# Performance work log

Measured on AMD Instinct MI355X. Metric: run time of the kernel, lower is better.

The kernel has to match this reference:

```python
import jax, jax.numpy as jnp
import numpy as np

IUNITS = 64  # input channels; scale is sqrt(iunits), per the original code


def setup_inputs() -> dict:
    key = jax.random.key(0)
    ks = jax.random.split(key, 4)
    B, N, Cin, Cout = 16, 2048, 64, 128
    x = jax.random.normal(ks[0], (B, N, Cin), dtype=jnp.float32)
    # 0.05 scaling keeps naive exp/sum softmax in a sane numeric range
    Wq = jax.random.normal(ks[1], (Cin, Cout), dtype=jnp.float32) * 0.05
    Wk = jax.random.normal(ks[2], (Cin, Cout), dtype=jnp.float32) * 0.05
    Wv = jax.random.normal(ks[3], (Cin, Cout), dtype=jnp.float32) * 0.05
    bq = jnp.zeros((Cout,), dtype=jnp.float32)
    bk = jnp.zeros((Cout,), dtype=jnp.float32)
    bv = jnp.zeros((Cout,), dtype=jnp.float32)
    return {"x": x, "Wq": Wq, "bq": bq, "Wk": Wk, "bk": bk, "Wv": Wv, "bv": bv}


def reference(x, Wq, bq, Wk, bk, Wv, bv):
    # Dense projections with ReLU activation (as in the original Dense(..., activation='relu'))
    Q = jax.nn.relu(jnp.einsum('bnc,cd->bnd', x, Wq) + bq)  # [B,N,D]
    K = jax.nn.relu(jnp.einsum('bnc,cd->bnd', x, Wk) + bk)  # [B,N,D]
    V = jax.nn.relu(jnp.einsum('bnc,cd->bnd', x, Wv) + bv)  # [B,N,D]
    scale = jnp.sqrt(jnp.float32(IUNITS))  # NOTE: sqrt of INPUT units, per source
    qk = jnp.einsum('bnd,bmd->bnm', Q, K) / scale            # [B,N,N]
    # exp/sum softmax over last axis; jax.nn.softmax is the same math, stabilized
    wgts = jax.nn.softmax(qk, axis=-1)
    return jnp.einsum('bnm,bmd->bnd', wgts, V)               # [B,N,D]
```

## Files before the change

### kernel.cpp

```cpp
#include <hip/hip_runtime.h>

typedef unsigned short u16;
typedef unsigned int u32;
typedef __bf16 bf16x8 __attribute__((ext_vector_type(8)));
typedef float f32x16 __attribute__((ext_vector_type(16)));
typedef u32 u32x4 __attribute__((ext_vector_type(4)));

#define QSCALE 0.18033688011112042f

__device__ __forceinline__ u16 bfbits(float f) {
  __bf16 h = (__bf16)f;
  return __builtin_bit_cast(u16, h);
}
__device__ __forceinline__ u32 pack2(float lo, float hi) {
  return (u32)bfbits(lo) | ((u32)bfbits(hi) << 16);
}
__device__ __forceinline__ void pl32swap(u32& a, u32& b) {
  asm volatile("v_permlane32_swap_b32 %0, %1" : "+v"(a), "+v"(b));
}
__device__ __forceinline__ void gload_lds16(const void* g, void* l) {
  __builtin_amdgcn_global_load_lds(
      (const __attribute__((address_space(1))) void*)g,
      (__attribute__((address_space(3))) void*)l, 16, 0, 0);
}

__global__ __launch_bounds__(256) void kv_proj_kernel(
    const float* __restrict__ x,
    const float* __restrict__ Wk, const float* __restrict__ bk,
    const float* __restrict__ Wv, const float* __restrict__ bv,
    u16* __restrict__ Kb, u16* __restrict__ VbT) {
  __shared__ __align__(16) u16 xs[64 * 64];
  const int t = threadIdx.x, w = t >> 6, lane = t & 63;
  const int ql = lane & 31, hi = lane >> 5;
  const int ws_ = w & 1;
  const int th = w >> 1;
  const size_t rg0 = (size_t)blockIdx.x * 64;

  {
    const float4* xsrc = reinterpret_cast<const float4*>(x + rg0 * 64);
#pragma unroll
    for (int i = 0; i < 4; ++i) {
      int idx = t + i * 256;
      int row = idx >> 4, c4 = idx & 15;
      float4 v = xsrc[idx];
      char* p = reinterpret_cast<char*>(xs) + row * 128 + ((c4 * 8) ^ ((row & 7) << 4));
      *reinterpret_cast<uint2*>(p) = make_uint2(pack2(v.x, v.y), pack2(v.z, v.w));
    }
  }
  __syncthreads();

  bf16x8 xf[4];
  {
    const int row = ws_ * 32 + ql;
    const char* base = reinterpret_cast<const char*>(xs) + row * 128;
    const int swz = (row & 7) << 4;
#pragma unroll
    for (int j = 0; j < 4; ++j)
      xf[j] = *reinterpret_cast<const bf16x8*>(base + ((j * 32 + hi * 16) ^ swz));
  }

  const float* W = th ? Wv : Wk;
  const float* bb = th ? bv : bk;
  const int b = (int)(rg0 >> 11);
  const int n0 = (int)(rg0 & 2047);

#pragma unroll
  for (int ct = 0; ct < 4; ++ct) {
    const int c = ct * 32 + ql;
    f32x16 acc;
#pragma unroll
    for (int i2 = 0; i2 < 16; ++i2) acc[i2] = 0.f;
#pragma unroll
    for (int j = 0; j < 4; ++j) {
      u32 wp[4];
#pragma unroll
      for (int e2 = 0; e2 < 4; ++e2) {
        float w0 = W[(j * 16 + hi * 8 + 2 * e2) * 128 + c];
        float w1 = W[(j * 16 + hi * 8 + 2 * e2 + 1) * 128 + c];
        wp[e2] = pack2(w0, w1);
      }
      u32x4 ww; ww.x = wp[0]; ww.y = wp[1]; ww.z = wp[2]; ww.w = wp[3];
      const bf16x8 wf = __builtin_bit_cast(bf16x8, ww);
      acc = __builtin_amdgcn_mfma_f32_32x32x16_bf16(xf[j], wf, acc, 0, 0, 0);
    }
    const float bias = bb[c];
    if (th == 0) {
#pragma unroll
      for (int reg = 0; reg < 16; ++reg) {
        const int i = (reg & 3) + 8 * (reg >> 2) + 4 * hi;
        Kb[(rg0 + ws_ * 32 + i) * 128 + c] = bfbits(fmaxf(acc[reg] + bias, 0.f));
      }
    } else {
      u16* vrow = VbT + ((size_t)(b * 128 + c)) * 2048;
#pragma unroll
      for (int g2 = 0; g2 < 4; ++g2) {
        u32 p0 = pack2(fmaxf(acc[4 * g2 + 0] + bias, 0.f),
                       fmaxf(acc[4 * g2 + 1] + bias, 0.f));
        u32 p1 = pack2(fmaxf(acc[4 * g2 + 2] + bias, 0.f),
                       fmaxf(acc[4 * g2 + 3] + bias, 0.f));
        const int n = n0 + ws_ * 32 + 8 * g2 + 4 * hi;
        *reinterpret_cast<uint2*>(vrow + n) = make_uint2(p0, p1);
      }
    }
  }
}

__global__ __launch_bounds__(256) void attn_kernel(
    const float* __restrict__ x,
    const float* __restrict__ Wq, const float* __restrict__ bq,
    const u16* __restrict__ Kb, const u16* __restrict__ VbT,
    float* __restrict__ out) {
  __shared__ __align__(16) char smem[65536];

  const int bid = ((int)blockIdx.x & 7) * 64 + ((int)blockIdx.x >> 3);
  const int b = bid >> 5;
  const int qt = bid & 31;
  const int t = threadIdx.x, w = t >> 6, lane = t & 63;
  const int ql = lane & 31, hi = lane >> 5;
  const size_t rg0 = (size_t)b * 2048 + qt * 64;
  const int sw = (ql & 7) << 4;

  {
    u16* xs = reinterpret_cast<u16*>(smem + 16384);
    const float4* xsrc = reinterpret_cast<const float4*>(x + rg0 * 64);
#pragma unroll
    for (int i = 0; i < 4; ++i) {
      int idx = t + i * 256;
      int row = idx >> 4, c4 = idx & 15;
      float4 v = xsrc[idx];
      char* p = reinterpret_cast<char*>(xs) + row * 128 + ((c4 * 8) ^ ((row & 7) << 4));
      *reinterpret_cast<uint2*>(p) = make_uint2(pack2(v.x, v.y), pack2(v.z, v.w));
    }
    __syncthreads();

    const int ws_ = w & 1;
    bf16x8 xf[4];
    {
      const int row = ws_ * 32 + ql;
      const char* base = reinterpret_cast<const char*>(xs) + row * 128;
      const int swz = (row & 7) << 4;
#pragma unroll
      for (int j = 0; j < 4; ++j)
        xf[j] = *reinterpret_cast<const bf16x8*>(base + ((j * 32 + hi * 16) ^ swz));
    }
#pragma unroll
    for (int u = 0; u < 2; ++u) {
      const int ct = (w >> 1) * 2 + u;
      const int c = ct * 32 + ql;
      f32x16 acc;
#pragma unroll
      for (int i2 = 0; i2 < 16; ++i2) acc[i2] = 0.f;
#pragma unroll
      for (int j = 0; j < 4; ++j) {
        u32 wp[4];
#pragma unroll
        for (int e2 = 0; e2 < 4; ++e2) {
          float w0 = Wq[(j * 16 + hi * 8 + 2 * e2) * 128 + c];
          float w1 = Wq[(j * 16 + hi * 8 + 2 * e2 + 1) * 128 + c];
          wp[e2] = pack2(w0, w1);
        }
        u32x4 ww; ww.x = wp[0]; ww.y = wp[1]; ww.z = wp[2]; ww.w = wp[3];
        const bf16x8 wf = __builtin_bit_cast(bf16x8, ww);
        acc = __builtin_amdgcn_mfma_f32_32x32x16_bf16(xf[j], wf, acc, 0, 0, 0);
      }
      const float bias = bq[c];
#pragma unroll
      for (int reg = 0; reg < 16; ++reg) {
        const int i = (reg & 3) + 8 * (reg >> 2) + 4 * hi;
        const int r = ws_ * 32 + i;
        *reinterpret_cast<u16*>(smem + r * 256 + ((2 * c) ^ ((r & 7) << 4))) =
            bfbits(fmaxf(acc[reg] + bias, 0.f) * QSCALE);
      }
    }
  }
  __syncthreads();

  const int qw = w >> 1, par = w & 1;
  const int q0 = qt * 64 + qw * 32;
  bf16x8 qf[8];
  {
    const int r = qw * 32 + ql;
    const char* base = smem + r * 256;
    const int swz = (r & 7) << 4;
#pragma unroll
    for (int f = 0; f < 8; ++f)
      qf[f] = *reinterpret_cast<const bf16x8*>(base + ((f * 32 + hi * 16) ^ swz));
  }
  __syncthreads();

  f32x16 Oacc[4], lacc;
#pragma unroll
  for (int i = 0; i < 16; ++i) {
    Oacc[0][i] = 0.f; Oacc[1][i] = 0.f; Oacc[2][i] = 0.f; Oacc[3][i] = 0.f;
    lacc[i] = 0.f;
  }
  u32x4 ow; ow.x = ow.y = ow.z = ow.w = 0x3F803F80u;
  const bf16x8 ones = __builtin_bit_cast(bf16x8, ow);

  const u16* Kbase = Kb + (size_t)b * 2048 * 128;
  const u16* Vbase = VbT + (size_t)b * 128 * 2048;

  const u16* kgp[4]; const u16* vgp[4];
  int ldso[4];
#pragma unroll
  for (int i = 0; i < 4; ++i) {
    const int Lb = (w * 4 + i) * 1024 + lane * 16;
    ldso[i] = (w * 4 + i) * 1024;
    const int kr = Lb >> 8;
    const int ks = ((Lb >> 4) & 15) ^ (kr & 7);
    kgp[i] = Kbase + kr * 128 + ks * 8;
    const int vr = Lb >> 7;
    const int vs = ((Lb >> 4) & 7) ^ (vr & 7);
    vgp[i] = Vbase + (size_t)vr * 2048 + vs * 8;
  }

#pragma unroll
  for (int i = 0; i < 4; ++i) {
    gload_lds16(kgp[i], smem + ldso[i]);
    gload_lds16(vgp[i], smem + 32768 + ldso[i]);
  }
  __syncthreads();

  for (int ss = 0; ss < 32; ++ss) {
    const int cur = ss & 1;
    if (ss < 31) {
      const size_t ko = (size_t)(ss + 1) * 8192;
      const int vo = (ss + 1) * 64;
      const int bo = (cur ^ 1) * 16384;
#pragma unroll
      for (int i = 0; i < 4; ++i) {
        gload_lds16(kgp[i] + ko, smem + bo + ldso[i]);
        gload_lds16(vgp[i] + vo, smem + 32768 + bo + ldso[i]);
      }
    }
    const char* kb0 = smem + cur * 16384;
    const char* vb0 = smem + 32768 + cur * 16384;

    f32x16 s0;
#pragma unroll
    for (int i = 0; i < 16; ++i) s0[i] = 0.f;
    const char* kbp = kb0 + (par * 32 + ql) * 256;
    __builtin_amdgcn_s_setprio(1);
#pragma unroll
    for (int f = 0; f < 8; ++f) {
      bf16x8 k0 = *reinterpret_cast<const bf16x8*>(kbp + ((f * 32 + hi * 16) ^ sw));
      s0 = __builtin_amdgcn_mfma_f32_32x32x16_bf16(k0, qf[f], s0, 0, 0, 0);
    }
    __builtin_amdgcn_s_setprio(0);

    u32 pk[8];
#pragma unroll
    for (int m = 0; m < 8; ++m)
      pk[m] = pack2(__builtin_amdgcn_exp2f(s0[2 * m]),
                    __builtin_amdgcn_exp2f(s0[2 * m + 1]));

    __builtin_amdgcn_s_setprio(1);
#pragma unroll
    for (int s2 = 0; s2 < 2; ++s2) {
      u32 X0 = pk[4 * s2 + 0], X1 = pk[4 * s2 + 1];
      u32 Y0 = pk[4 * s2 + 2], Y1 = pk[4 * s2 + 3];
      pl32swap(X0, Y0);
      pl32swap(X1, Y1);
      u32x4 frw; frw.x = X0; frw.y = X1; frw.z = Y0; frw.w = Y1;
      const bf16x8 pf = __builtin_bit_cast(bf16x8, frw);
      lacc = __builtin_amdgcn_mfma_f32_32x32x16_bf16(pf, ones, lacc, 0, 0, 0);
#pragma unroll
      for (int dt = 0; dt < 4; ++dt) {
        const int dr = dt * 32 + ql;
        bf16x8 vf = *reinterpret_cast<const bf16x8*>(
            vb0 + dr * 128 + ((par * 64 + s2 * 32 + hi * 16) ^ ((dr & 7) << 4)));
        Oacc[dt] = __builtin_amdgcn_mfma_f32_32x32x16_bf16(pf, vf, Oacc[dt], 0, 0, 0);
      }
    }
    __builtin_amdgcn_s_setprio(0);

    __syncthreads();
  }

  float* Ost = reinterpret_cast<float*>(smem);
  float* Lst = reinterpret_cast<float*>(smem + 32768);
  if (par == 1) {
#pragma unroll
    for (int reg = 0; reg < 16; ++reg) {
      const int qr = (reg & 3) + 8 * (reg >> 2) + 4 * hi;
      float* orow = Ost + (size_t)(qw * 32 + qr) * 128 + ql;
#pragma unroll
      for (int dt = 0; dt < 4; ++dt) orow[dt * 32] = Oacc[dt][reg];
      if (ql == 0) Lst[qw * 32 + qr] = lacc[reg];
    }
  }
  __syncthreads();
  if (par == 0) {
#pragma unroll
    for (int reg = 0; reg < 16; ++reg) {
      const int qr = (reg & 3) + 8 * (reg >> 2) + 4 * hi;
      const float inv = 1.f / (lacc[reg] + Lst[qw * 32 + qr]);
      const float* prow = Ost + (size_t)(qw * 32 + qr) * 128 + ql;
      float* orow = out + ((size_t)(b * 2048 + q0 + qr)) * 128 + ql;
#pragma unroll
      for (int dt = 0; dt < 4; ++dt)
        orow[dt * 32] = (Oacc[dt][reg] + prow[dt * 32]) * inv;
    }
  }
}

extern "C" void kernel_launch(void* const* d_in, const int* in_sizes, int n_in,
                              void* d_out, int out_size, void* d_ws, size_t ws_size,
                              hipStream_t stream) {
  const float* x  = (const float*)d_in[0];
  const float* Wq = (const float*)d_in[1];
  const float* bq = (const float*)d_in[2];
  const float* Wk = (const float*)d_in[3];
  const float* bk = (const float*)d_in[4];
  const float* Wv = (const float*)d_in[5];
  const float* bv = (const float*)d_in[6];
  float* out = (float*)d_out;

  u16* Kb  = (u16*)d_ws;
  u16* VbT = Kb + (size_t)16 * 2048 * 128;

  kv_proj_kernel<<<512, 256, 0, stream>>>(x, Wk, bk, Wv, bv, Kb, VbT);
  attn_kernel<<<512, 256, 0, stream>>>(x, Wq, bq, Kb, VbT, out);
}
```

Baseline: 70.26 us.

## Load K tiles straight into registers and split QK accumulation chains

K tiles are no longer staged in LDS with async global-to-LDS loads. Each lane loads its own K row fragments from global memory into registers, double-buffered across iterations by unrolling the loop by two. This roughly halves the LDS footprint and removes the LDS reads for K. The QK^T MFMA chain is split into two independent accumulators that are summed before the exp, shortening the dependency chain. The trade-offs are more VGPRs and less coalesced, latency-exposed global K loads issued one step ahead.

```diff
diff --git a/kernel.cpp b/kernel.cpp
--- a/kernel.cpp
+++ b/kernel.cpp
@@ -110,7 +110,7 @@
     const float* __restrict__ Wq, const float* __restrict__ bq,
     const u16* __restrict__ Kb, const u16* __restrict__ VbT,
     float* __restrict__ out) {
-  __shared__ __align__(16) char smem[65536];
+  __shared__ __align__(16) char smem[33280];
 
   const int bid = ((int)blockIdx.x & 7) * 64 + ((int)blockIdx.x >> 3);
   const int b = bid >> 5;
@@ -197,85 +197,84 @@
   u32x4 ow; ow.x = ow.y = ow.z = ow.w = 0x3F803F80u;
   const bf16x8 ones = __builtin_bit_cast(bf16x8, ow);
 
-  const u16* Kbase = Kb + (size_t)b * 2048 * 128;
   const u16* Vbase = VbT + (size_t)b * 128 * 2048;
-
-  const u16* kgp[4]; const u16* vgp[4];
+  const u16* Krow = Kb + (size_t)b * 2048 * 128 + (par * 32 + ql) * 128 + hi * 8;
+
+  const u16* vgp[4];
   int ldso[4];
 #pragma unroll
   for (int i = 0; i < 4; ++i) {
     const int Lb = (w * 4 + i) * 1024 + lane * 16;
     ldso[i] = (w * 4 + i) * 1024;
-    const int kr = Lb >> 8;
-    const int ks = ((Lb >> 4) & 15) ^ (kr & 7);
-    kgp[i] = Kbase + kr * 128 + ks * 8;
     const int vr = Lb >> 7;
     const int vs = ((Lb >> 4) & 7) ^ (vr & 7);
     vgp[i] = Vbase + (size_t)vr * 2048 + vs * 8;
   }
 
-#pragma unroll
-  for (int i = 0; i < 4; ++i) {
-    gload_lds16(kgp[i], smem + ldso[i]);
-    gload_lds16(vgp[i], smem + 32768 + ldso[i]);
-  }
-  __syncthreads();
-
-  for (int ss = 0; ss < 32; ++ss) {
-    const int cur = ss & 1;
-    if (ss < 31) {
-      const size_t ko = (size_t)(ss + 1) * 8192;
-      const int vo = (ss + 1) * 64;
-      const int bo = (cur ^ 1) * 16384;
-#pragma unroll
-      for (int i = 0; i < 4; ++i) {
-        gload_lds16(kgp[i] + ko, smem + bo + ldso[i]);
-        gload_lds16(vgp[i] + vo, smem + 32768 + bo + ldso[i]);
-      }
-    }
-    const char* kb0 = smem + cur * 16384;
-    const char* vb0 = smem + 32768 + cur * 16384;
-
-    f32x16 s0;
-#pragma unroll
-    for (int i = 0; i < 16; ++i) s0[i] = 0.f;
-    const char* kbp = kb0 + (par * 32 + ql) * 256;
-    __builtin_amdgcn_s_setprio(1);
-#pragma unroll
-    for (int f = 0; f < 8; ++f) {
-      bf16x8 k0 = *reinterpret_cast<const bf16x8*>(kbp + ((f * 32 + hi * 16) ^ sw));
-      s0 = __builtin_amdgcn_mfma_f32_32x32x16_bf16(k0, qf[f], s0, 0, 0, 0);
-    }
-    __builtin_amdgcn_s_setprio(0);
-
-    u32 pk[8];
-#pragma unroll
-    for (int m = 0; m < 8; ++m)
-      pk[m] = pack2(__builtin_amdgcn_exp2f(s0[2 * m]),
-                    __builtin_amdgcn_exp2f(s0[2 * m + 1]));
-
-    __builtin_amdgcn_s_setprio(1);
-#pragma unroll
-    for (int s2 = 0; s2 < 2; ++s2) {
-      u32 X0 = pk[4 * s2 + 0], X1 = pk[4 * s2 + 1];
-      u32 Y0 = pk[4 * s2 + 2], Y1 = pk[4 * s2 + 3];
-      pl32swap(X0, Y0);
-      pl32swap(X1, Y1);
-      u32x4 frw; frw.x = X0; frw.y = X1; frw.z = Y0; frw.w = Y1;
-      const bf16x8 pf = __builtin_bit_cast(bf16x8, frw);
-      lacc = __builtin_amdgcn_mfma_f32_32x32x16_bf16(pf, ones, lacc, 0, 0, 0);
-#pragma unroll
-      for (int dt = 0; dt < 4; ++dt) {
-        const int dr = dt * 32 + ql;
-        bf16x8 vf = *reinterpret_cast<const bf16x8*>(
-            vb0 + dr * 128 + ((par * 64 + s2 * 32 + hi * 16) ^ ((dr & 7) << 4)));
-        Oacc[dt] = __builtin_amdgcn_mfma_f32_32x32x16_bf16(pf, vf, Oacc[dt], 0, 0, 0);
-      }
-    }
-    __builtin_amdgcn_s_setprio(0);
-
-    __syncthreads();
-  }
+  bf16x8 kA[8], kB[8];
+#pragma unroll
+  for (int i = 0; i < 4; ++i) gload_lds16(vgp[i], smem + ldso[i]);
+#pragma unroll
+  for (int f = 0; f < 8; ++f)
+    kA[f] = *reinterpret_cast<const bf16x8*>(Krow + f * 16);
+  __syncthreads();
+
+#define ATTN_BODY(SS, CUR, KC, KN)                                             \
+  {                                                                            \
+    if ((SS) < 31) {                                                           \
+      const int vo = ((SS) + 1) * 64;                                          \
+      const int bo = ((CUR) ^ 1) * 16384;                                      \
+      _Pragma("unroll")                                                        \
+      for (int i = 0; i < 4; ++i) gload_lds16(vgp[i] + vo, smem + bo + ldso[i]); \
+      const u16* kp = Krow + (size_t)((SS) + 1) * 8192;                        \
+      _Pragma("unroll")                                                        \
+      for (int f = 0; f < 8; ++f)                                              \
+        KN[f] = *reinterpret_cast<const bf16x8*>(kp + f * 16);                 \
+    }                                                                          \
+    const char* vb0 = smem + (CUR) * 16384;                                    \
+    f32x16 s0a, s0b;                                                           \
+    _Pragma("unroll")                                                          \
+    for (int i = 0; i < 16; ++i) { s0a[i] = 0.f; s0b[i] = 0.f; }               \
+    __builtin_amdgcn_s_setprio(1);                                             \
+    _Pragma("unroll")                                                          \
+    for (int f2 = 0; f2 < 4; ++f2) {                                           \
+      s0a = __builtin_amdgcn_mfma_f32_32x32x16_bf16(KC[2 * f2], qf[2 * f2], s0a, 0, 0, 0); \
+      s0b = __builtin_amdgcn_mfma_f32_32x32x16_bf16(KC[2 * f2 + 1], qf[2 * f2 + 1], s0b, 0, 0, 0); \
+    }                                                                          \
+    __builtin_amdgcn_s_setprio(0);                                             \
+    u32 pk[8];                                                                 \
+    _Pragma("unroll")                                                          \
+    for (int m = 0; m < 8; ++m)                                                \
+      pk[m] = pack2(__builtin_amdgcn_exp2f(s0a[2 * m] + s0b[2 * m]),           \
+                    __builtin_amdgcn_exp2f(s0a[2 * m + 1] + s0b[2 * m + 1]));  \
+    __builtin_amdgcn_s_setprio(1);                                             \
+    _Pragma("unroll")                                                          \
+    for (int s2 = 0; s2 < 2; ++s2) {                                           \
+      u32 X0 = pk[4 * s2 + 0], X1 = pk[4 * s2 + 1];                            \
+      u32 Y0 = pk[4 * s2 + 2], Y1 = pk[4 * s2 + 3];                            \
+      pl32swap(X0, Y0);                                                        \
+      pl32swap(X1, Y1);                                                        \
+      u32x4 frw; frw.x = X0; frw.y = X1; frw.z = Y0; frw.w = Y1;               \
+      const bf16x8 pf = __builtin_bit_cast(bf16x8, frw);                       \
+      lacc = __builtin_amdgcn_mfma_f32_32x32x16_bf16(pf, ones, lacc, 0, 0, 0); \
+      _Pragma("unroll")                                                        \
+      for (int dt = 0; dt < 4; ++dt) {                                         \
+        const int dr = dt * 32 + ql;                                           \
+        bf16x8 vf = *reinterpret_cast<const bf16x8*>(                          \
+            vb0 + dr * 128 + ((par * 64 + s2 * 32 + hi * 16) ^ ((dr & 7) << 4))); \
+        Oacc[dt] = __builtin_amdgcn_mfma_f32_32x32x16_bf16(pf, vf, Oacc[dt], 0, 0, 0); \
+      }                                                                        \
+    }                                                                          \
+    __builtin_amdgcn_s_setprio(0);                                             \
+    __syncthreads();                                                           \
+  }
+
+  for (int ss2 = 0; ss2 < 16; ++ss2) {
+    const int ss = 2 * ss2;
+    ATTN_BODY(ss, 0, kA, kB)
+    ATTN_BODY(ss + 1, 1, kB, kA)
+  }
+#undef ATTN_BODY
 
   float* Ost = reinterpret_cast<float*>(smem);
   float* Lst = reinterpret_cast<float*>(smem + 32768);
```

After: 115.0 us. 63.6% more time.

## Restructure K/V prefetch: K two ahead, V single-buffered, split QK accumulators

Applied to the files above, without the earlier changes.

Changes the attention loop's LDS pipeline so K tiles are prefetched two iterations ahead in a double buffer, while V uses one buffer that is refilled right after the PV MFMAs. Explicit vmcnt waits and raw barriers replace the single __syncthreads. LDS shrinks from 64KB to 48KB, which may allow more resident blocks. The QK^T MFMA chain is split into two independent accumulators to shorten the dependency chain. In exchange there are more barriers per iteration, V loads are exposed to the softmax phase, and the hand-counted vmcnt values are fragile to get right.

```diff
diff --git a/kernel.cpp b/kernel.cpp
--- a/kernel.cpp
+++ b/kernel.cpp
@@ -23,6 +23,9 @@
       (const __attribute__((address_space(1))) void*)g,
       (__attribute__((address_space(3))) void*)l, 16, 0, 0);
 }
+#define VMCNT(N) do { asm volatile("s_waitcnt vmcnt(" #N ")" ::: "memory"); \
+                      __builtin_amdgcn_sched_barrier(0); } while (0)
+#define RBAR() __builtin_amdgcn_s_barrier()
 
 __global__ __launch_bounds__(256) void kv_proj_kernel(
     const float* __restrict__ x,
@@ -110,7 +113,7 @@
     const float* __restrict__ Wq, const float* __restrict__ bq,
     const u16* __restrict__ Kb, const u16* __restrict__ VbT,
     float* __restrict__ out) {
-  __shared__ __align__(16) char smem[65536];
+  __shared__ __align__(16) char smem[49152];
 
   const int bid = ((int)blockIdx.x & 7) * 64 + ((int)blockIdx.x >> 3);
   const int b = bid >> 5;
@@ -213,46 +216,42 @@
     const int vs = ((Lb >> 4) & 7) ^ (vr & 7);
     vgp[i] = Vbase + (size_t)vr * 2048 + vs * 8;
   }
-
-#pragma unroll
-  for (int i = 0; i < 4; ++i) {
-    gload_lds16(kgp[i], smem + ldso[i]);
-    gload_lds16(vgp[i], smem + 32768 + ldso[i]);
-  }
-  __syncthreads();
+  char* const Vb0 = smem + 32768;
+
+#pragma unroll
+  for (int i = 0; i < 4; ++i) gload_lds16(kgp[i], smem + ldso[i]);
+#pragma unroll
+  for (int i = 0; i < 4; ++i) gload_lds16(vgp[i], Vb0 + ldso[i]);
+  __syncthreads();
+#pragma unroll
+  for (int i = 0; i < 4; ++i) gload_lds16(kgp[i] + 8192, smem + 16384 + ldso[i]);
 
   for (int ss = 0; ss < 32; ++ss) {
     const int cur = ss & 1;
-    if (ss < 31) {
-      const size_t ko = (size_t)(ss + 1) * 8192;
-      const int vo = (ss + 1) * 64;
-      const int bo = (cur ^ 1) * 16384;
-#pragma unroll
-      for (int i = 0; i < 4; ++i) {
-        gload_lds16(kgp[i] + ko, smem + bo + ldso[i]);
-        gload_lds16(vgp[i] + vo, smem + 32768 + bo + ldso[i]);
-      }
-    }
     const char* kb0 = smem + cur * 16384;
-    const char* vb0 = smem + 32768 + cur * 16384;
-
-    f32x16 s0;
-#pragma unroll
-    for (int i = 0; i < 16; ++i) s0[i] = 0.f;
+
+    f32x16 s0a, s0b;
+#pragma unroll
+    for (int i = 0; i < 16; ++i) { s0a[i] = 0.f; s0b[i] = 0.f; }
     const char* kbp = kb0 + (par * 32 + ql) * 256;
     __builtin_amdgcn_s_setprio(1);
 #pragma unroll
-    for (int f = 0; f < 8; ++f) {
-      bf16x8 k0 = *reinterpret_cast<const bf16x8*>(kbp + ((f * 32 + hi * 16) ^ sw));
-      s0 = __builtin_amdgcn_mfma_f32_32x32x16_bf16(k0, qf[f], s0, 0, 0, 0);
+    for (int f2 = 0; f2 < 4; ++f2) {
+      bf16x8 k0 = *reinterpret_cast<const bf16x8*>(kbp + (((2 * f2) * 32 + hi * 16) ^ sw));
+      bf16x8 k1 = *reinterpret_cast<const bf16x8*>(kbp + (((2 * f2 + 1) * 32 + hi * 16) ^ sw));
+      s0a = __builtin_amdgcn_mfma_f32_32x32x16_bf16(k0, qf[2 * f2], s0a, 0, 0, 0);
+      s0b = __builtin_amdgcn_mfma_f32_32x32x16_bf16(k1, qf[2 * f2 + 1], s0b, 0, 0, 0);
     }
     __builtin_amdgcn_s_setprio(0);
 
     u32 pk[8];
 #pragma unroll
     for (int m = 0; m < 8; ++m)
-      pk[m] = pack2(__builtin_amdgcn_exp2f(s0[2 * m]),
-                    __builtin_amdgcn_exp2f(s0[2 * m + 1]));
+      pk[m] = pack2(__builtin_amdgcn_exp2f(s0a[2 * m] + s0b[2 * m]),
+                    __builtin_amdgcn_exp2f(s0a[2 * m + 1] + s0b[2 * m + 1]));
+
+    if (ss < 31) { VMCNT(4); } else { VMCNT(0); }
+    RBAR();
 
     __builtin_amdgcn_s_setprio(1);
 #pragma unroll
@@ -268,14 +267,30 @@
       for (int dt = 0; dt < 4; ++dt) {
         const int dr = dt * 32 + ql;
         bf16x8 vf = *reinterpret_cast<const bf16x8*>(
-            vb0 + dr * 128 + ((par * 64 + s2 * 32 + hi * 16) ^ ((dr & 7) << 4)));
+            Vb0 + dr * 128 + ((par * 64 + s2 * 32 + hi * 16) ^ ((dr & 7) << 4)));
         Oacc[dt] = __builtin_amdgcn_mfma_f32_32x32x16_bf16(pf, vf, Oacc[dt], 0, 0, 0);
       }
     }
     __builtin_amdgcn_s_setprio(0);
 
-    __syncthreads();
-  }
+    RBAR();
+
+    if (ss < 31) {
+      const int vo = (ss + 1) * 64;
+#pragma unroll
+      for (int i = 0; i < 4; ++i) gload_lds16(vgp[i] + vo, Vb0 + ldso[i]);
+    }
+    if (ss < 30) {
+      const size_t ko = (size_t)(ss + 2) * 8192;
+#pragma unroll
+      for (int i = 0; i < 4; ++i) gload_lds16(kgp[i] + ko, smem + cur * 16384 + ldso[i]);
+    }
+
+    if (ss < 30) { VMCNT(8); } else if (ss == 30) { VMCNT(4); } else { VMCNT(0); }
+    RBAR();
+  }
+
+  __syncthreads();
 
   float* Ost = reinterpret_cast<float*>(smem);
   float* Lst = reinterpret_cast<float*>(smem + 32768);
```

Result: slower. 72.03 us (+2.5%).

## Split QK accumulation chains, precompute LDS offsets, reverse KV order for odd tiles

Applied to the files above, without the earlier changes.

Breaks the serial 8-MFMA QK^T dependency chain into two independent accumulators that are summed before exp2, shortening the per-tile latency. LDS read offsets for K and V fragments are precomputed once outside the loop. Odd query tiles now walk the KV tiles in reverse order, presumably to spread L2/HBM accesses across workgroups. The s_setprio hints are removed. The cost is extra VGPRs for the second accumulator and offset arrays, which may lower occupancy.

```diff
diff --git a/kernel.cpp b/kernel.cpp
--- a/kernel.cpp
+++ b/kernel.cpp
@@ -214,47 +214,60 @@
     vgp[i] = Vbase + (size_t)vr * 2048 + vs * 8;
   }
 
-#pragma unroll
-  for (int i = 0; i < 4; ++i) {
-    gload_lds16(kgp[i], smem + ldso[i]);
-    gload_lds16(vgp[i], smem + 32768 + ldso[i]);
+  int kread[8], vread[8];
+#pragma unroll
+  for (int f = 0; f < 8; ++f)
+    kread[f] = (par * 32 + ql) * 256 + ((f * 32 + hi * 16) ^ sw);
+#pragma unroll
+  for (int s2 = 0; s2 < 2; ++s2)
+#pragma unroll
+    for (int dt = 0; dt < 4; ++dt) {
+      const int dr = dt * 32 + ql;
+      vread[s2 * 4 + dt] = dr * 128 + ((par * 64 + s2 * 32 + hi * 16) ^ ((dr & 7) << 4));
+    }
+
+  const int revq = qt & 1;
+  {
+    const int kt0 = revq ? 31 : 0;
+#pragma unroll
+    for (int i = 0; i < 4; ++i) {
+      gload_lds16(kgp[i] + (size_t)kt0 * 8192, smem + ldso[i]);
+      gload_lds16(vgp[i] + kt0 * 64, smem + 32768 + ldso[i]);
+    }
   }
   __syncthreads();
 
   for (int ss = 0; ss < 32; ++ss) {
     const int cur = ss & 1;
     if (ss < 31) {
-      const size_t ko = (size_t)(ss + 1) * 8192;
-      const int vo = (ss + 1) * 64;
+      const int ktn = revq ? (30 - ss) : (ss + 1);
       const int bo = (cur ^ 1) * 16384;
 #pragma unroll
       for (int i = 0; i < 4; ++i) {
-        gload_lds16(kgp[i] + ko, smem + bo + ldso[i]);
-        gload_lds16(vgp[i] + vo, smem + 32768 + bo + ldso[i]);
+        gload_lds16(kgp[i] + (size_t)ktn * 8192, smem + bo + ldso[i]);
+        gload_lds16(vgp[i] + ktn * 64, smem + 32768 + bo + ldso[i]);
       }
     }
     const char* kb0 = smem + cur * 16384;
     const char* vb0 = smem + 32768 + cur * 16384;
 
-    f32x16 s0;
-#pragma unroll
-    for (int i = 0; i < 16; ++i) s0[i] = 0.f;
-    const char* kbp = kb0 + (par * 32 + ql) * 256;
-    __builtin_amdgcn_s_setprio(1);
-#pragma unroll
-    for (int f = 0; f < 8; ++f) {
-      bf16x8 k0 = *reinterpret_cast<const bf16x8*>(kbp + ((f * 32 + hi * 16) ^ sw));
-      s0 = __builtin_amdgcn_mfma_f32_32x32x16_bf16(k0, qf[f], s0, 0, 0, 0);
-    }
-    __builtin_amdgcn_s_setprio(0);
+    f32x16 s0a, s0b;
+#pragma unroll
+    for (int i = 0; i < 16; ++i) { s0a[i] = 0.f; s0b[i] = 0.f; }
+#pragma unroll
+    for (int f2 = 0; f2 < 4; ++f2) {
+      bf16x8 k0 = *reinterpret_cast<const bf16x8*>(kb0 + kread[2 * f2]);
+      bf16x8 k1 = *reinterpret_cast<const bf16x8*>(kb0 + kread[2 * f2 + 1]);
+      s0a = __builtin_amdgcn_mfma_f32_32x32x16_bf16(k0, qf[2 * f2], s0a, 0, 0, 0);
+      s0b = __builtin_amdgcn_mfma_f32_32x32x16_bf16(k1, qf[2 * f2 + 1], s0b, 0, 0, 0);
+    }
 
     u32 pk[8];
 #pragma unroll
     for (int m = 0; m < 8; ++m)
-      pk[m] = pack2(__builtin_amdgcn_exp2f(s0[2 * m]),
-                    __builtin_amdgcn_exp2f(s0[2 * m + 1]));
-
-    __builtin_amdgcn_s_setprio(1);
+      pk[m] = pack2(__builtin_amdgcn_exp2f(s0a[2 * m] + s0b[2 * m]),
+                    __builtin_amdgcn_exp2f(s0a[2 * m + 1] + s0b[2 * m + 1]));
+
 #pragma unroll
     for (int s2 = 0; s2 < 2; ++s2) {
       u32 X0 = pk[4 * s2 + 0], X1 = pk[4 * s2 + 1];
@@ -266,13 +279,10 @@
       lacc = __builtin_amdgcn_mfma_f32_32x32x16_bf16(pf, ones, lacc, 0, 0, 0);
 #pragma unroll
       for (int dt = 0; dt < 4; ++dt) {
-        const int dr = dt * 32 + ql;
-        bf16x8 vf = *reinterpret_cast<const bf16x8*>(
-            vb0 + dr * 128 + ((par * 64 + s2 * 32 + hi * 16) ^ ((dr & 7) << 4)));
+        bf16x8 vf = *reinterpret_cast<const bf16x8*>(vb0 + vread[s2 * 4 + dt]);
         Oacc[dt] = __builtin_amdgcn_mfma_f32_32x32x16_bf16(pf, vf, Oacc[dt], 0, 0, 0);
       }
     }
-    __builtin_amdgcn_s_setprio(0);
 
     __syncthreads();
   }
```

Result: slower. 90.69 us (+29.1%).
